# Kernel optimization log

Hardware: AMD Instinct MI355X
Metric: run time of the kernel (lower is better)

Reference implementation:

```python
import jax, jax.numpy as jnp
import numpy as np

NUM_HEADS = 32
HEAD_DIM = 64
ROPE_THETA = 10000.0


def _rope_cos_sin(position_ids, head_dim, theta):
    # inv_freq: [head_dim/2]
    half = head_dim // 2
    inv_freq = 1.0 / (theta ** (jnp.arange(0, half, dtype=jnp.float32) * 2.0 / head_dim))
    angles = position_ids.astype(jnp.float32)[..., None] * inv_freq  # [B,S,half]
    return jnp.cos(angles), jnp.sin(angles)


def _apply_rope(x, cos, sin):
    # x: [B,S,H,hd]; cos/sin: [B,S,half] -> broadcast over heads (rotate-half, Llama style)
    half = x.shape[-1] // 2
    x1, x2 = x[..., :half], x[..., half:]
    c = cos[:, :, None, :]
    s = sin[:, :, None, :]
    return jnp.concatenate([x1 * c - x2 * s, x2 * c + x1 * s], axis=-1)


def setup_inputs() -> dict:
    key = jax.random.key(0)
    ks = jax.random.split(key, 8)
    B, S, D = 2, 2048, 2048
    hidden_states = jax.random.normal(ks[0], (B, S, D), dtype=jnp.float32)
    # causal additive mask (is_causal=False in IpexSDP; mask carries causality)
    causal = jnp.tril(jnp.ones((S, S), dtype=jnp.bool_))
    attention_mask = jnp.where(causal, 0.0, -1e9).astype(jnp.float32)[None, None, :, :]
    attention_mask = jnp.broadcast_to(attention_mask, (B, 1, S, S))
    position_ids = jnp.broadcast_to(jnp.arange(S, dtype=jnp.int64)[None, :], (B, S))
    scale = 0.02
    qkv_w = jax.random.normal(ks[1], (3, D, D), dtype=jnp.float32) * scale
    qkv_b = jax.random.normal(ks[2], (3, D), dtype=jnp.float32) * scale
    o_w = jax.random.normal(ks[3], (D, D), dtype=jnp.float32) * scale
    o_b = jax.random.normal(ks[4], (D,), dtype=jnp.float32) * scale
    residual = jax.random.normal(ks[5], (B, S, D), dtype=jnp.float32)
    return {
        'hidden_states': hidden_states,
        'attention_mask': attention_mask,
        'position_ids': position_ids,
        'qkv_w': qkv_w,
        'qkv_b': qkv_b,
        'o_w': o_w,
        'o_b': o_b,
        'residual': residual,
    }


def reference(hidden_states, attention_mask, position_ids, qkv_w, qkv_b, o_w, o_b, residual):
    B, S, D = hidden_states.shape
    H, hd = NUM_HEADS, HEAD_DIM
    # fused QKV projection (weights stored transposed: x @ W), matching mm_qkv_out
    qkv = jnp.einsum('bsd,tde->tbse', hidden_states, qkv_w) + qkv_b[:, None, None, :]
    q = qkv[0].reshape(B, S, H, hd)
    k = qkv[1].reshape(B, S, H, hd)
    v = qkv[2].reshape(B, S, H, hd)
    cos, sin = _rope_cos_sin(position_ids, hd, ROPE_THETA)
    q = _apply_rope(q, cos, sin)
    k = _apply_rope(k, cos, sin)
    scale = 1.0 / jnp.sqrt(jnp.asarray(hd, dtype=hidden_states.dtype))
    # [B,H,S,S]
    scores = jnp.einsum('bqhd,bkhd->bhqk', q, k) * scale + attention_mask
    probs = jax.nn.softmax(scores, axis=-1)
    attn = jnp.einsum('bhqk,bkhd->bqhd', probs, v).reshape(B, S, D)
    # o-proj fused with bias + residual add (matmul_add_add)
    out = attn @ o_w + o_b + residual
    return out
```

## Files before the change

kernel.cpp:

```cpp
#include <hip/hip_runtime.h>
#include <stdint.h>
#include <stdio.h>

#define D_MODEL 2048
#define SEQ     2048
#define NHEADS  32
#define HDIM    64
#define BATCH   2
#define BH      (BATCH * NHEADS)
#define GK      2048

typedef unsigned short u16;
typedef unsigned int   u32;
typedef __attribute__((ext_vector_type(8))) short short8;
typedef __attribute__((ext_vector_type(4))) short s16x4;
typedef __attribute__((ext_vector_type(4))) float f32x4;
typedef __attribute__((ext_vector_type(4))) u32   u32x4;
typedef __attribute__((ext_vector_type(2))) u32   u32x2;

__device__ __forceinline__ float bf2f(u16 x) {
  union { u32 u; float f; } c; c.u = ((u32)x) << 16; return c.f;
}
__device__ __forceinline__ u16 f2bf(float f) {
  union { float f; u32 u; } c; c.f = f;
  u32 u = c.u;
  return (u16)((u + 0x7FFFu + ((u >> 16) & 1u)) >> 16);
}
__device__ __forceinline__ u32 fbits(float f) {
  union { float f; u32 u; } c; c.f = f; return c.u;
}

typedef const __attribute__((address_space(1))) u32* gas_t;
typedef __attribute__((address_space(3))) u32* las_t;
__device__ __forceinline__ void gll16(const void* g, void* l) {
  __builtin_amdgcn_global_load_lds((gas_t)g, (las_t)l, 16, 0, 0);
}

__device__ __forceinline__ void swiz_mn(int pid, int nx, int& mtile, int& ntile) {
  int chunk = 8 * nx;
  int grp = pid / chunk, loc = pid - grp * chunk;
  mtile = grp * 8 + (loc & 7);
  ntile = loc >> 3;
}

__global__ __launch_bounds__(256) void cvt_k(const float* __restrict__ in,
                                             u16* __restrict__ out) {
  int id = blockIdx.x * 256 + threadIdx.x;
  f32x4 v = *(const f32x4*)&in[(size_t)id * 4];
  alignas(8) u16 o[4];
#pragma unroll
  for (int j = 0; j < 4; j++) o[j] = f2bf(v[j]);
  *(u32x2*)&out[(size_t)id * 4] = *(const u32x2*)o;
}

__global__ __launch_bounds__(256) void transpose_cvt_k(const float* __restrict__ qkv_w,
                                                       const float* __restrict__ o_w,
                                                       u16* __restrict__ outT) {
  __shared__ u16 tile[64][72];
  const int z = blockIdx.z;
  const float* inz = (z < 3) ? qkv_w + (size_t)z * D_MODEL * D_MODEL : o_w;
  u16* outz = outT + (size_t)z * D_MODEL * D_MODEL;
  const int r0 = blockIdx.y * 64, c0 = blockIdx.x * 64;
  const int t = threadIdx.x;
  const int lrow = t >> 4, lcol4 = (t & 15) * 4;
#pragma unroll
  for (int i = 0; i < 4; i++) {
    int r = lrow + i * 16;
    f32x4 v = *(const f32x4*)&inz[(size_t)(r0 + r) * D_MODEL + (c0 + lcol4)];
#pragma unroll
    for (int j = 0; j < 4; j++) tile[r][lcol4 + j] = f2bf(v[j]);
  }
  __syncthreads();
  const int row = t >> 3, col8 = (t & 7) * 8;
#pragma unroll
  for (int i = 0; i < 2; i++) {
    int r = row + i * 32;
    alignas(16) u16 vals[8];
#pragma unroll
    for (int j = 0; j < 8; j++) vals[j] = tile[col8 + j][r];
    *(u32x4*)&outz[(size_t)(c0 + r) * D_MODEL + (r0 + col8)] = *(const u32x4*)vals;
  }
}

__device__ __forceinline__ void gemm128(const u16* __restrict__ A, const u16* __restrict__ BT,
                                        int m0, int n0, u16* As, u16* Bs, f32x4 acc[4][4]) {
  const int t = threadIdx.x;
  const int lane = t & 63, w = t >> 6;
  const int quad = lane >> 4, l16 = lane & 15;
  const int wr = w >> 1, wc = w & 1;
  const int ldr = lane >> 2, ldc = (lane & 3) * 8;
#pragma unroll
  for (int mt = 0; mt < 4; mt++)
#pragma unroll
    for (int nt = 0; nt < 4; nt++)
#pragma unroll
      for (int i = 0; i < 4; i++) acc[mt][nt][i] = 0.0f;

  for (int k0 = 0; k0 < GK; k0 += 32) {
    __syncthreads();
#pragma unroll
    for (int i = 0; i < 2; i++) {
      int rbase = w * 32 + i * 16;
      gll16(&A[(size_t)(m0 + rbase + ldr) * GK + k0 + ldc], &As[rbase * 32]);
      gll16(&BT[(size_t)(n0 + rbase + ldr) * GK + k0 + ldc], &Bs[rbase * 32]);
    }
    __syncthreads();
    short8 af[4], bf[4];
#pragma unroll
    for (int mt = 0; mt < 4; mt++)
      af[mt] = *(const short8*)&As[(wr * 64 + mt * 16 + l16) * 32 + quad * 8];
#pragma unroll
    for (int nt = 0; nt < 4; nt++)
      bf[nt] = *(const short8*)&Bs[(wc * 64 + nt * 16 + l16) * 32 + quad * 8];
#pragma unroll
    for (int mt = 0; mt < 4; mt++)
#pragma unroll
      for (int nt = 0; nt < 4; nt++)
        acc[mt][nt] = __builtin_amdgcn_mfma_f32_16x16x32_bf16(af[mt], bf[nt], acc[mt][nt], 0, 0, 0);
  }
}

__global__ __launch_bounds__(256) void qkv_gemm_k(const u16* __restrict__ A, const u16* __restrict__ BT,
                                                  const float* __restrict__ bias,
                                                  u16* __restrict__ Qb, u16* __restrict__ Kb,
                                                  u16* __restrict__ Vbt) {
  __shared__ u16 As[128 * 32], Bs[128 * 32];
  f32x4 acc[4][4];
  int mtile, ntile;
  swiz_mn(blockIdx.x, 48, mtile, ntile);
  const int m0 = mtile * 128, n0 = ntile * 128;
  gemm128(A, BT, m0, n0, As, Bs, acc);
  const int t = threadIdx.x, lane = t & 63, quad = lane >> 4, l16 = lane & 15;
  const int w = t >> 6, wr = w >> 1, wc = w & 1;
  const int tsel = n0 >> 11;

  if (tsel < 2) {
    u16* dst = tsel ? Kb : Qb;
#pragma unroll
    for (int p = 0; p < 2; p++) {
      int nlo = n0 + wc * 64 + p * 16 + l16;
      float blo = bias[nlo], bhi = bias[nlo + 32];
      int j = p * 16 + l16;
      float inv = __expf((float)j * -0.28782313662425572f);
      int h = (nlo & 2047) >> 6;
#pragma unroll
      for (int mt = 0; mt < 4; mt++) {
#pragma unroll
        for (int r = 0; r < 4; r++) {
          int m = m0 + wr * 64 + mt * 16 + quad * 4 + r;
          int b = m >> 11, s = m & (SEQ - 1);
          float sn, cs;
          __sincosf((float)s * inv, &sn, &cs);
          float x1 = acc[mt][p][r] + blo;
          float x2 = acc[mt][p + 2][r] + bhi;
          size_t base = ((size_t)((b * NHEADS + h) * SEQ + s)) * HDIM;
          dst[base + j]      = f2bf(x1 * cs - x2 * sn);
          dst[base + j + 32] = f2bf(x2 * cs + x1 * sn);
        }
      }
    }
  } else {
#pragma unroll
    for (int nt = 0; nt < 4; nt++) {
      int n = n0 + wc * 64 + nt * 16 + l16;
      float bv = bias[n];
      int e = n & 2047, h = e >> 6, d = e & 63;
#pragma unroll
      for (int mt = 0; mt < 4; mt++) {
        int m0r = m0 + wr * 64 + mt * 16 + quad * 4;
        int b = m0r >> 11, s0 = m0r & (SEQ - 1);
        alignas(8) u16 o4[4];
#pragma unroll
        for (int r = 0; r < 4; r++) o4[r] = f2bf(acc[mt][nt][r] + bv);
        *(u32x2*)&Vbt[((size_t)((b * NHEADS + h) * HDIM + d)) * SEQ + s0] = *(const u32x2*)o4;
      }
    }
  }
}

__global__ __launch_bounds__(256) void oproj_gemm_k(const u16* __restrict__ A, const u16* __restrict__ BT,
                                                    const float* __restrict__ bias,
                                                    const float* __restrict__ resid,
                                                    float* __restrict__ out) {
  __shared__ u16 As[128 * 32], Bs[128 * 32];
  f32x4 acc[4][4];
  int mtile, ntile;
  swiz_mn(blockIdx.x, 16, mtile, ntile);
  const int m0 = mtile * 128, n0 = ntile * 128;
  gemm128(A, BT, m0, n0, As, Bs, acc);
  const int t = threadIdx.x, lane = t & 63, quad = lane >> 4, l16 = lane & 15;
  const int w = t >> 6, wr = w >> 1, wc = w & 1;
#pragma unroll
  for (int nt = 0; nt < 4; nt++) {
    int n = n0 + wc * 64 + nt * 16 + l16;
    float bv = bias[n];
#pragma unroll
    for (int mt = 0; mt < 4; mt++) {
#pragma unroll
      for (int r = 0; r < 4; r++) {
        int m = m0 + wr * 64 + mt * 16 + quad * 4 + r;
        size_t oi = (size_t)m * D_MODEL + n;
        out[oi] = acc[mt][nt][r] + bv + resid[oi];
      }
    }
  }
}

__global__ __launch_bounds__(256, 2) void attn_k(const u16* __restrict__ Qb,
                                                 const u16* __restrict__ Kb,
                                                 const u16* __restrict__ Vbt,
                                                 u16* __restrict__ attn) {
  __shared__ u16 smem[128 * 72];
  u16* Ks = smem;
  u16* Vt = smem + 64 * 72;
  const int blk = blockIdx.x;
  const int bh = blk & 63, pi = blk >> 6;
  const int b = bh >> 5, h = bh & 31;
  const int t = threadIdx.x, w = t >> 6, lane = t & 63, quad = lane >> 4, l16 = lane & 15;
  const int qbT[2] = { pi * 128, (15 - pi) * 128 };
  const int qwT[2] = { qbT[0] + w * 32, qbT[1] + w * 32 };
  const size_t bho = (size_t)bh * SEQ * HDIM;
  const size_t vbo = (size_t)bh * HDIM * SEQ;
  const int kend = qbT[1] + 128;

  short8 qf[2][2][2];
#pragma unroll
  for (int Ti = 0; Ti < 2; Ti++)
#pragma unroll
    for (int qt = 0; qt < 2; qt++)
#pragma unroll
      for (int kd = 0; kd < 2; kd++) {
        short8 v = *(const short8*)&Qb[bho + (size_t)(qwT[Ti] + qt * 16 + l16) * HDIM + kd * 32 + quad * 8];
#pragma unroll
        for (int i = 0; i < 8; i++) {
          float f = bf2f((u16)v[i]) * 0.125f;
          v[i] = (short)f2bf(f);
        }
        qf[Ti][qt][kd] = v;
      }

  f32x4 Oacc[2][4][2];
  float mrow[2][2] = {{-1e30f, -1e30f}, {-1e30f, -1e30f}};
  float lrow[2][2] = {{0.0f, 0.0f}, {0.0f, 0.0f}};
#pragma unroll
  for (int Ti = 0; Ti < 2; Ti++)
#pragma unroll
    for (int dt = 0; dt < 4; dt++)
#pragma unroll
      for (int qt = 0; qt < 2; qt++)
#pragma unroll
        for (int i = 0; i < 4; i++) Oacc[Ti][dt][qt][i] = 0.0f;

  const int srow = t >> 3, sc8 = (t & 7) * 8;
  u32x4 kreg[2], vreg[2];

#pragma unroll
  for (int j = 0; j < 2; j++) {
    kreg[j] = *(const u32x4*)&Kb[bho + (size_t)(srow + j * 32) * HDIM + sc8];
    vreg[j] = *(const u32x4*)&Vbt[vbo + (size_t)(srow + j * 32) * SEQ + sc8];
  }
#pragma unroll
  for (int j = 0; j < 2; j++) {
    *(u32x4*)&Ks[(srow + j * 32) * 72 + sc8] = kreg[j];
    *(u32x4*)&Vt[(srow + j * 32) * 72 + sc8] = vreg[j];
  }
  __syncthreads();

  for (int key0 = 0; key0 < kend; key0 += 64) {
    const int nxt = key0 + 64;
    if (nxt < kend) {
#pragma unroll
      for (int j = 0; j < 2; j++) {
        kreg[j] = *(const u32x4*)&Kb[bho + (size_t)(nxt + srow + j * 32) * HDIM + sc8];
        vreg[j] = *(const u32x4*)&Vbt[vbo + (size_t)(srow + j * 32) * SEQ + nxt + sc8];
      }
    }
#pragma unroll
    for (int Ti = 0; Ti < 2; Ti++) {
      const int qw = qwT[Ti];
      if (key0 <= qw + 31) {
        const int lim = qw + 31 - key0;
        int nkt = (lim >> 4) + 1; if (nkt > 4) nkt = 4;
        f32x4 sacc[4][2];
#pragma unroll
        for (int kt = 0; kt < 4; kt++) {
          if (kt < nkt) {
            short8 kf0 = *(const short8*)&Ks[(kt * 16 + l16) * 72 + quad * 8];
            short8 kf1 = *(const short8*)&Ks[(kt * 16 + l16) * 72 + 32 + quad * 8];
#pragma unroll
            for (int qt = 0; qt < 2; qt++) {
              f32x4 z = {0.0f, 0.0f, 0.0f, 0.0f};
              z = __builtin_amdgcn_mfma_f32_16x16x32_bf16(kf0, qf[Ti][qt][0], z, 0, 0, 0);
              z = __builtin_amdgcn_mfma_f32_16x16x32_bf16(kf1, qf[Ti][qt][1], z, 0, 0, 0);
              sacc[kt][qt] = z;
            }
          }
        }
        if (key0 + 63 > qw) {
#pragma unroll
          for (int qt = 0; qt < 2; qt++) {
            int qrow = qw + qt * 16 + l16;
#pragma unroll
            for (int kt = 0; kt < 4; kt++)
              if (kt < nkt)
#pragma unroll
                for (int r = 0; r < 4; r++)
                  if (key0 + kt * 16 + quad * 4 + r > qrow) sacc[kt][qt][r] = -1e30f;
          }
        }
        float alpha[2];
#pragma unroll
        for (int qt = 0; qt < 2; qt++) {
          float mx = -1e30f;
#pragma unroll
          for (int kt = 0; kt < 4; kt++)
            if (kt < nkt)
#pragma unroll
              for (int r = 0; r < 4; r++) mx = fmaxf(mx, sacc[kt][qt][r]);
          mx = fmaxf(mx, __shfl_xor(mx, 16));
          mx = fmaxf(mx, __shfl_xor(mx, 32));
          float mnew = fmaxf(mrow[Ti][qt], mx);
          alpha[qt] = __expf(mrow[Ti][qt] - mnew);
          mrow[Ti][qt] = mnew;
          float rsum = 0.0f;
#pragma unroll
          for (int kt = 0; kt < 4; kt++)
            if (kt < nkt)
#pragma unroll
              for (int r = 0; r < 4; r++) {
                float pv = __expf(sacc[kt][qt][r] - mnew);
                sacc[kt][qt][r] = pv;
                rsum += pv;
              }
          rsum += __shfl_xor(rsum, 16);
          rsum += __shfl_xor(rsum, 32);
          lrow[Ti][qt] = lrow[Ti][qt] * alpha[qt] + rsum;
        }
#pragma unroll
        for (int dt = 0; dt < 4; dt++)
#pragma unroll
          for (int qt = 0; qt < 2; qt++)
#pragma unroll
            for (int r = 0; r < 4; r++) Oacc[Ti][dt][qt][r] *= alpha[qt];
#pragma unroll
        for (int kt = 0; kt < 4; kt++) {
          if (kt < nkt) {
            s16x4 pk[2];
#pragma unroll
            for (int qt = 0; qt < 2; qt++) {
              u32 a0 = fbits(sacc[kt][qt][0]) + 0x8000u;
              u32 a1 = fbits(sacc[kt][qt][1]) + 0x8000u;
              u32 a2 = fbits(sacc[kt][qt][2]) + 0x8000u;
              u32 a3 = fbits(sacc[kt][qt][3]) + 0x8000u;
              union { u32 u[2]; s16x4 s; } pc;
              pc.u[0] = __builtin_amdgcn_perm(a1, a0, 0x07060302u);
              pc.u[1] = __builtin_amdgcn_perm(a3, a2, 0x07060302u);
              pk[qt] = pc.s;
            }
            s16x4 vf[4];
#pragma unroll
            for (int dt = 0; dt < 4; dt++)
              vf[dt] = *(const s16x4*)&Vt[(dt * 16 + l16) * 72 + kt * 16 + quad * 4];
#pragma unroll
            for (int dt = 0; dt < 4; dt++)
#pragma unroll
              for (int qt = 0; qt < 2; qt++)
                Oacc[Ti][dt][qt] = __builtin_amdgcn_mfma_f32_16x16x16bf16_1k(vf[dt], pk[qt], Oacc[Ti][dt][qt], 0, 0, 0);
          }
        }
      }
    }
    __syncthreads();
    if (nxt < kend) {
#pragma unroll
      for (int j = 0; j < 2; j++) {
        *(u32x4*)&Ks[(srow + j * 32) * 72 + sc8] = kreg[j];
        *(u32x4*)&Vt[(srow + j * 32) * 72 + sc8] = vreg[j];
      }
      __syncthreads();
    }
  }

#pragma unroll
  for (int Ti = 0; Ti < 2; Ti++) {
    float invl[2] = {1.0f / lrow[Ti][0], 1.0f / lrow[Ti][1]};
#pragma unroll
    for (int dt = 0; dt < 4; dt++)
#pragma unroll
      for (int qt = 0; qt < 2; qt++)
#pragma unroll
        for (int r = 0; r < 4; r++)
          smem[(w * 32 + qt * 16 + l16) * 72 + dt * 16 + quad * 4 + r] =
              f2bf(Oacc[Ti][dt][qt][r] * invl[qt]);
    __syncthreads();
#pragma unroll
    for (int ii = 0; ii < 4; ii++) {
      int chunk = t + ii * 256;
      int row = chunk >> 3, g = chunk & 7;
      *(u32x4*)&attn[((size_t)(b * SEQ + qbT[Ti] + row)) * D_MODEL + h * 64 + g * 8] =
          *(const u32x4*)&smem[row * 72 + g * 8];
    }
    __syncthreads();
  }
}

extern "C" void kernel_launch(void* const* d_in, const int* in_sizes, int n_in,
                              void* d_out, int out_size, void* d_ws, size_t ws_size,
                              hipStream_t stream) {
  (void)in_sizes; (void)n_in; (void)out_size;
  const float* hidden = (const float*)d_in[0];
  const float* qkv_w = (const float*)d_in[3];
  const float* qkv_b = (const float*)d_in[4];
  const float* o_w   = (const float*)d_in[5];
  const float* o_b   = (const float*)d_in[6];
  const float* resid = (const float*)d_in[7];
  float* out = (float*)d_out;

  u16* ws = (u16*)d_ws;
  size_t off = 0;
  u16* hidb  = ws + off; off += (size_t)BATCH * SEQ * D_MODEL;
  u16* qkvT  = ws + off; off += (size_t)3 * D_MODEL * D_MODEL;
  u16* owT   = ws + off; off += (size_t)D_MODEL * D_MODEL;
  u16* Qb    = ws + off; off += (size_t)BH * SEQ * HDIM;
  u16* Kb    = ws + off; off += (size_t)BH * SEQ * HDIM;
  u16* Vbt   = ws + off; off += (size_t)BH * SEQ * HDIM;
  u16* attnb = ws + off; off += (size_t)BATCH * SEQ * D_MODEL;
  if (ws_size < off * sizeof(u16)) {
    fprintf(stderr, "kernel_launch: workspace too small: need %zu bytes, have %zu\n",
            off * sizeof(u16), ws_size);
    return;
  }
  (void)owT;

  cvt_k<<<(BATCH * SEQ * D_MODEL) / (4 * 256), 256, 0, stream>>>(hidden, hidb);
  transpose_cvt_k<<<dim3(32, 32, 4), 256, 0, stream>>>(qkv_w, o_w, qkvT);
  qkv_gemm_k<<<48 * 32, 256, 0, stream>>>(hidb, qkvT, qkv_b, Qb, Kb, Vbt);
  attn_k<<<BH * 8, 256, 0, stream>>>(Qb, Kb, Vbt, attnb);
  oproj_gemm_k<<<16 * 32, 256, 0, stream>>>(attnb, owT, o_b, resid, out);
}
```

Baseline: 443.1 us.

## Rewrite QKV GEMM with 256x256 tiles, double-buffered swizzled LDS and interleaved loads

Replaces the 128x128 QKV projection GEMM with a 512-thread kernel computing 256x256 output tiles at K-step 64. LDS is double-buffered and XOR-swizzled, and global-to-LDS loads for the next tiles are interleaved with four MFMA phases under s_setprio and barriers. The aim is more data reuse per LDS byte, fewer bank conflicts and loads overlapped with compute. The cost is 128KB of LDS and one block per CU, and the grid shrinks to 384 blocks, which may not fill all CUs evenly. The RoPE and V-transpose epilogue is adapted to the new fragment layout.

```diff
diff --git a/kernel.cpp b/kernel.cpp
--- a/kernel.cpp
+++ b/kernel.cpp
@@ -120,20 +120,136 @@
   }
 }
 
-__global__ __launch_bounds__(256) void qkv_gemm_k(const u16* __restrict__ A, const u16* __restrict__ BT,
-                                                  const float* __restrict__ bias,
-                                                  u16* __restrict__ Qb, u16* __restrict__ Kb,
-                                                  u16* __restrict__ Vbt) {
-  __shared__ u16 As[128 * 32], Bs[128 * 32];
-  f32x4 acc[4][4];
+
+__device__ __forceinline__ short8 lds_frag(const u16* tile, int row, int kh, int quad) {
+  int off = row * 128 + ((kh * 64 + quad * 16) ^ ((row & 4) << 3));
+  return *(const short8*)((const char*)tile + off);
+}
+
+__device__ __forceinline__ void stage_half(const u16* __restrict__ src, int rowbase, int k0,
+                                           u16* tile, int h, int w, int srl, int scol) {
+  u16* ldsb = tile + h * (128 * 64);
+  const u16* g0 = &src[(size_t)(rowbase + h * 128 + srl) * GK + k0 + scol];
+  const u16* g1 = &src[(size_t)(rowbase + h * 128 + srl + 8) * GK + k0 + scol];
+  gll16(g0, (char*)ldsb + w * 2048);
+  gll16(g1, (char*)ldsb + w * 2048 + 1024);
+}
+
+__global__ __launch_bounds__(512, 1) void qkv_gemm256_k(const u16* __restrict__ A,
+                                                        const u16* __restrict__ BT,
+                                                        const float* __restrict__ bias,
+                                                        u16* __restrict__ Qb, u16* __restrict__ Kb,
+                                                        u16* __restrict__ Vbt) {
+  __shared__ u16 As[2][256 * 64];
+  __shared__ u16 Bs[2][256 * 64];
+  const int t = threadIdx.x, w = t >> 6, lane = t & 63;
+  const int quad = lane >> 4, l16 = lane & 15;
+  const int wr = w >> 2, wc = w & 3;
   int mtile, ntile;
-  swiz_mn(blockIdx.x, 48, mtile, ntile);
-  const int m0 = mtile * 128, n0 = ntile * 128;
-  gemm128(A, BT, m0, n0, As, Bs, acc);
-  const int t = threadIdx.x, lane = t & 63, quad = lane >> 4, l16 = lane & 15;
-  const int w = t >> 6, wr = w >> 1, wc = w & 1;
+  swiz_mn(blockIdx.x, 24, mtile, ntile);
+  const int m0 = mtile * 256, n0 = ntile * 256;
+  const int srl = w * 16 + (lane >> 3);
+  const int scol = ((((lane & 7) * 16) ^ (((lane >> 5) & 1) << 5))) >> 1;
+
+  f32x4 acc[8][4];
+#pragma unroll
+  for (int mf = 0; mf < 8; mf++)
+#pragma unroll
+    for (int nf = 0; nf < 4; nf++)
+#pragma unroll
+      for (int i = 0; i < 4; i++) acc[mf][nf][i] = 0.0f;
+
+  const int NT = GK / 64;
+  stage_half(A, m0, 0, As[0], 0, w, srl, scol);
+  stage_half(A, m0, 0, As[0], 1, w, srl, scol);
+  stage_half(BT, n0, 0, Bs[0], 0, w, srl, scol);
+  stage_half(BT, n0, 0, Bs[0], 1, w, srl, scol);
+  stage_half(A, m0, 64, As[1], 0, w, srl, scol);
+  stage_half(A, m0, 64, As[1], 1, w, srl, scol);
+  asm volatile("s_waitcnt vmcnt(4)" ::: "memory");
+  __builtin_amdgcn_s_barrier();
+
+  for (int kt = 0; kt < NT; kt++) {
+    const int cur = kt & 1;
+    const u16* Ac = As[cur];
+    const u16* Bc = Bs[cur];
+    short8 af[8][2], bf[4][2];
+#pragma unroll
+    for (int mf = 0; mf < 4; mf++) {
+      af[mf][0] = lds_frag(Ac, wr * 128 + mf * 16 + l16, 0, quad);
+      af[mf][1] = lds_frag(Ac, wr * 128 + mf * 16 + l16, 1, quad);
+    }
+#pragma unroll
+    for (int nf = 0; nf < 2; nf++) {
+      bf[nf][0] = lds_frag(Bc, wc * 64 + nf * 16 + l16, 0, quad);
+      bf[nf][1] = lds_frag(Bc, wc * 64 + nf * 16 + l16, 1, quad);
+    }
+    if (kt + 1 < NT) stage_half(BT, n0, (kt + 1) * 64, Bs[cur ^ 1], 0, w, srl, scol);
+    __builtin_amdgcn_s_barrier();
+    __builtin_amdgcn_s_setprio(1);
+#pragma unroll
+    for (int mf = 0; mf < 4; mf++)
+#pragma unroll
+      for (int nf = 0; nf < 2; nf++) {
+        acc[mf][nf] = __builtin_amdgcn_mfma_f32_16x16x32_bf16(af[mf][0], bf[nf][0], acc[mf][nf], 0, 0, 0);
+        acc[mf][nf] = __builtin_amdgcn_mfma_f32_16x16x32_bf16(af[mf][1], bf[nf][1], acc[mf][nf], 0, 0, 0);
+      }
+    __builtin_amdgcn_s_setprio(0);
+    __builtin_amdgcn_s_barrier();
+#pragma unroll
+    for (int mf = 4; mf < 8; mf++) {
+      af[mf][0] = lds_frag(Ac, wr * 128 + mf * 16 + l16, 0, quad);
+      af[mf][1] = lds_frag(Ac, wr * 128 + mf * 16 + l16, 1, quad);
+    }
+#pragma unroll
+    for (int nf = 2; nf < 4; nf++) {
+      bf[nf][0] = lds_frag(Bc, wc * 64 + nf * 16 + l16, 0, quad);
+      bf[nf][1] = lds_frag(Bc, wc * 64 + nf * 16 + l16, 1, quad);
+    }
+    if (kt + 1 < NT) stage_half(BT, n0, (kt + 1) * 64, Bs[cur ^ 1], 1, w, srl, scol);
+    __builtin_amdgcn_s_barrier();
+    __builtin_amdgcn_s_setprio(1);
+#pragma unroll
+    for (int mf = 4; mf < 8; mf++)
+#pragma unroll
+      for (int nf = 0; nf < 2; nf++) {
+        acc[mf][nf] = __builtin_amdgcn_mfma_f32_16x16x32_bf16(af[mf][0], bf[nf][0], acc[mf][nf], 0, 0, 0);
+        acc[mf][nf] = __builtin_amdgcn_mfma_f32_16x16x32_bf16(af[mf][1], bf[nf][1], acc[mf][nf], 0, 0, 0);
+      }
+    __builtin_amdgcn_s_setprio(0);
+    __builtin_amdgcn_s_barrier();
+    if (kt + 2 < NT) stage_half(A, m0, (kt + 2) * 64, As[cur], 0, w, srl, scol);
+    __builtin_amdgcn_s_barrier();
+    __builtin_amdgcn_s_setprio(1);
+#pragma unroll
+    for (int mf = 0; mf < 4; mf++)
+#pragma unroll
+      for (int nf = 2; nf < 4; nf++) {
+        acc[mf][nf] = __builtin_amdgcn_mfma_f32_16x16x32_bf16(af[mf][0], bf[nf][0], acc[mf][nf], 0, 0, 0);
+        acc[mf][nf] = __builtin_amdgcn_mfma_f32_16x16x32_bf16(af[mf][1], bf[nf][1], acc[mf][nf], 0, 0, 0);
+      }
+    __builtin_amdgcn_s_setprio(0);
+    __builtin_amdgcn_s_barrier();
+    if (kt + 2 < NT) stage_half(A, m0, (kt + 2) * 64, As[cur], 1, w, srl, scol);
+    __builtin_amdgcn_s_barrier();
+    __builtin_amdgcn_s_setprio(1);
+#pragma unroll
+    for (int mf = 4; mf < 8; mf++)
+#pragma unroll
+      for (int nf = 2; nf < 4; nf++) {
+        acc[mf][nf] = __builtin_amdgcn_mfma_f32_16x16x32_bf16(af[mf][0], bf[nf][0], acc[mf][nf], 0, 0, 0);
+        acc[mf][nf] = __builtin_amdgcn_mfma_f32_16x16x32_bf16(af[mf][1], bf[nf][1], acc[mf][nf], 0, 0, 0);
+      }
+    __builtin_amdgcn_s_setprio(0);
+    if (kt + 2 < NT) {
+      asm volatile("s_waitcnt vmcnt(4)" ::: "memory");
+    } else {
+      asm volatile("s_waitcnt vmcnt(0)" ::: "memory");
+    }
+    __builtin_amdgcn_s_barrier();
+  }
+
   const int tsel = n0 >> 11;
-
   if (tsel < 2) {
     u16* dst = tsel ? Kb : Qb;
 #pragma unroll
@@ -144,15 +260,15 @@
       float inv = __expf((float)j * -0.28782313662425572f);
       int h = (nlo & 2047) >> 6;
 #pragma unroll
-      for (int mt = 0; mt < 4; mt++) {
+      for (int mf = 0; mf < 8; mf++) {
 #pragma unroll
         for (int r = 0; r < 4; r++) {
-          int m = m0 + wr * 64 + mt * 16 + quad * 4 + r;
+          int m = m0 + wr * 128 + mf * 16 + quad * 4 + r;
           int b = m >> 11, s = m & (SEQ - 1);
           float sn, cs;
           __sincosf((float)s * inv, &sn, &cs);
-          float x1 = acc[mt][p][r] + blo;
-          float x2 = acc[mt][p + 2][r] + bhi;
+          float x1 = acc[mf][p][r] + blo;
+          float x2 = acc[mf][p + 2][r] + bhi;
           size_t base = ((size_t)((b * NHEADS + h) * SEQ + s)) * HDIM;
           dst[base + j]      = f2bf(x1 * cs - x2 * sn);
           dst[base + j + 32] = f2bf(x2 * cs + x1 * sn);
@@ -161,17 +277,17 @@
     }
   } else {
 #pragma unroll
-    for (int nt = 0; nt < 4; nt++) {
-      int n = n0 + wc * 64 + nt * 16 + l16;
+    for (int nf = 0; nf < 4; nf++) {
+      int n = n0 + wc * 64 + nf * 16 + l16;
       float bv = bias[n];
       int e = n & 2047, h = e >> 6, d = e & 63;
 #pragma unroll
-      for (int mt = 0; mt < 4; mt++) {
-        int m0r = m0 + wr * 64 + mt * 16 + quad * 4;
+      for (int mf = 0; mf < 8; mf++) {
+        int m0r = m0 + wr * 128 + mf * 16 + quad * 4;
         int b = m0r >> 11, s0 = m0r & (SEQ - 1);
         alignas(8) u16 o4[4];
 #pragma unroll
-        for (int r = 0; r < 4; r++) o4[r] = f2bf(acc[mt][nt][r] + bv);
+        for (int r = 0; r < 4; r++) o4[r] = f2bf(acc[mf][nf][r] + bv);
         *(u32x2*)&Vbt[((size_t)((b * NHEADS + h) * HDIM + d)) * SEQ + s0] = *(const u32x2*)o4;
       }
     }
@@ -434,7 +550,7 @@
 
   cvt_k<<<(BATCH * SEQ * D_MODEL) / (4 * 256), 256, 0, stream>>>(hidden, hidb);
   transpose_cvt_k<<<dim3(32, 32, 4), 256, 0, stream>>>(qkv_w, o_w, qkvT);
-  qkv_gemm_k<<<48 * 32, 256, 0, stream>>>(hidb, qkvT, qkv_b, Qb, Kb, Vbt);
+  qkv_gemm256_k<<<16 * 24, 512, 0, stream>>>(hidb, qkvT, qkv_b, Qb, Kb, Vbt);
   attn_k<<<BH * 8, 256, 0, stream>>>(Qb, Kb, Vbt, attnb);
   oproj_gemm_k<<<16 * 32, 256, 0, stream>>>(attnb, owT, o_b, resid, out);
 }
```

Result: no change. 443.8 us (+0.2%).

## Rewrite GEMMs as 128x256 tiles with triple-buffered async LDS pipeline

Applied to the files above, without the earlier changes.

Replaces the simple 128x128, K=32 double-sync GEMM loop with a 128x256 tile on 512 threads that triple-buffers K=64 slabs through global_load_lds. It uses XOR-swizzled LDS layout, hand-scheduled ds_read_b128 with explicit waitcnt, and register double-buffered fragments. MFMA sections run at raised priority. The aim is to hide global and LDS latency and cut barrier overhead in the QKV and output projections. In exchange it uses much more LDS, allows one block per CU, and launches fewer blocks, which may leave the output projection underfilling the GPU.

```diff
diff --git a/kernel.cpp b/kernel.cpp
--- a/kernel.cpp
+++ b/kernel.cpp
@@ -9,6 +9,7 @@
 #define BATCH   2
 #define BH      (BATCH * NHEADS)
 #define GK      2048
+#define NT      (GK / 64)
 
 typedef unsigned short u16;
 typedef unsigned int   u32;
@@ -35,6 +36,17 @@
 __device__ __forceinline__ void gll16(const void* g, void* l) {
   __builtin_amdgcn_global_load_lds((gas_t)g, (las_t)l, 16, 0, 0);
 }
+__device__ __forceinline__ u32 lds_addr(const void* p) {
+  return (u32)(size_t)(const __attribute__((address_space(3))) void*)p;
+}
+template <int OFF>
+__device__ __forceinline__ short8 ds_read128o(u32 addr) {
+  short8 r;
+  asm volatile("ds_read_b128 %0, %1 offset:%2" : "=v"(r) : "v"(addr), "i"(OFF));
+  return r;
+}
+
+#define SBAR0 __builtin_amdgcn_sched_barrier(0)
 
 __device__ __forceinline__ void swiz_mn(int pid, int nx, int& mtile, int& ntile) {
   int chunk = 8 * nx;
@@ -82,58 +94,127 @@
   }
 }
 
-__device__ __forceinline__ void gemm128(const u16* __restrict__ A, const u16* __restrict__ BT,
-                                        int m0, int n0, u16* As, u16* Bs, f32x4 acc[4][4]) {
-  const int t = threadIdx.x;
-  const int lane = t & 63, w = t >> 6;
+
+__device__ __forceinline__ void stage_half(const u16* __restrict__ src, int rowbase, int k0,
+                                           u16* tile, int h, int w, int srl, int scol) {
+  u16* ldsb = tile + h * (128 * 64);
+  const u16* g0 = &src[(size_t)(rowbase + h * 128 + srl) * GK + k0 + scol];
+  const u16* g1 = &src[(size_t)(rowbase + h * 128 + srl + 8) * GK + k0 + scol];
+  gll16(g0, (char*)ldsb + w * 2048);
+  gll16(g1, (char*)ldsb + w * 2048 + 1024);
+}
+
+__device__ __forceinline__ void rd8(short8 dst[4][2], u32 base, u32 cq0, u32 cq1) {
+  u32 b0 = base + cq0, b1 = base + cq1;
+  dst[0][0] = ds_read128o<0>(b0);    dst[0][1] = ds_read128o<0>(b1);
+  dst[1][0] = ds_read128o<2048>(b0); dst[1][1] = ds_read128o<2048>(b1);
+  dst[2][0] = ds_read128o<4096>(b0); dst[2][1] = ds_read128o<4096>(b1);
+  dst[3][0] = ds_read128o<6144>(b0); dst[3][1] = ds_read128o<6144>(b1);
+}
+
+template <int NFLO>
+__device__ __forceinline__ void mfma_half(const short8 afc[4][2], const short8 bfc[4][2],
+                                          f32x4 acc[4][4]) {
+  __builtin_amdgcn_s_setprio(1);
+#pragma unroll
+  for (int mf = 0; mf < 4; mf++)
+#pragma unroll
+    for (int nf = NFLO; nf < NFLO + 2; nf++) {
+      acc[mf][nf] = __builtin_amdgcn_mfma_f32_16x16x32_bf16(afc[mf][0], bfc[nf][0], acc[mf][nf], 0, 0, 0);
+      acc[mf][nf] = __builtin_amdgcn_mfma_f32_16x16x32_bf16(afc[mf][1], bfc[nf][1], acc[mf][nf], 0, 0, 0);
+    }
+  __builtin_amdgcn_s_setprio(0);
+}
+
+#define KT_BODY(KT_, AFC, BFC, AFN, BFN)                                        \
+  do {                                                                           \
+    if ((KT_) + 1 < NT) rd8(AFN, asb + (u32)ri * (u32)(128 * 64 * 2) + rowA, cq0, cq1); \
+    if ((KT_) + 1 < NT) { asm volatile("s_waitcnt lgkmcnt(8)"); }                \
+    else                { asm volatile("s_waitcnt lgkmcnt(0)"); }                \
+    SBAR0;                                                                       \
+    mfma_half<0>(AFC, BFC, acc);                                                 \
+    if ((KT_) + 1 < NT) rd8(BFN, bsb + (u32)ri * (u32)(256 * 64 * 2) + rowB, cq0, cq1); \
+    SBAR0;                                                                       \
+    mfma_half<2>(AFC, BFC, acc);                                                 \
+    __builtin_amdgcn_s_barrier();                                                \
+    SBAR0;                                                                       \
+    if ((KT_) + 3 < NT) {                                                        \
+      const int k3_ = ((KT_) + 3) * 64;                                          \
+      stage_half(Ag, m0, k3_, AsB + si * (128 * 64), 0, w, srl, scol);           \
+      stage_half(Bg, n0, k3_, BsB + si * (256 * 64), 0, w, srl, scol);           \
+      stage_half(Bg, n0, k3_, BsB + si * (256 * 64), 1, w, srl, scol);           \
+      asm volatile("s_waitcnt vmcnt(6)");                                        \
+    } else {                                                                     \
+      asm volatile("s_waitcnt vmcnt(0)");                                        \
+    }                                                                            \
+    SBAR0;                                                                       \
+    __builtin_amdgcn_s_barrier();                                                \
+    SBAR0;                                                                       \
+    { int th_ = 3 - si - ri; si = ri; ri = th_; }                                \
+  } while (0)
+
+__device__ __forceinline__ void gemm_128x256(const u16* __restrict__ Ag,
+                                             const u16* __restrict__ Bg,
+                                             int m0, int n0,
+                                             u16* AsB, u16* BsB,
+                                             f32x4 acc[4][4]) {
+  const int t = threadIdx.x, w = t >> 6, lane = t & 63;
   const int quad = lane >> 4, l16 = lane & 15;
-  const int wr = w >> 1, wc = w & 1;
-  const int ldr = lane >> 2, ldc = (lane & 3) * 8;
-#pragma unroll
-  for (int mt = 0; mt < 4; mt++)
-#pragma unroll
-    for (int nt = 0; nt < 4; nt++)
-#pragma unroll
-      for (int i = 0; i < 4; i++) acc[mt][nt][i] = 0.0f;
-
-  for (int k0 = 0; k0 < GK; k0 += 32) {
-    __syncthreads();
-#pragma unroll
-    for (int i = 0; i < 2; i++) {
-      int rbase = w * 32 + i * 16;
-      gll16(&A[(size_t)(m0 + rbase + ldr) * GK + k0 + ldc], &As[rbase * 32]);
-      gll16(&BT[(size_t)(n0 + rbase + ldr) * GK + k0 + ldc], &Bs[rbase * 32]);
-    }
-    __syncthreads();
-    short8 af[4], bf[4];
-#pragma unroll
-    for (int mt = 0; mt < 4; mt++)
-      af[mt] = *(const short8*)&As[(wr * 64 + mt * 16 + l16) * 32 + quad * 8];
-#pragma unroll
-    for (int nt = 0; nt < 4; nt++)
-      bf[nt] = *(const short8*)&Bs[(wc * 64 + nt * 16 + l16) * 32 + quad * 8];
-#pragma unroll
-    for (int mt = 0; mt < 4; mt++)
-#pragma unroll
-      for (int nt = 0; nt < 4; nt++)
-        acc[mt][nt] = __builtin_amdgcn_mfma_f32_16x16x32_bf16(af[mt], bf[nt], acc[mt][nt], 0, 0, 0);
-  }
-}
-
-__global__ __launch_bounds__(256) void qkv_gemm_k(const u16* __restrict__ A, const u16* __restrict__ BT,
-                                                  const float* __restrict__ bias,
-                                                  u16* __restrict__ Qb, u16* __restrict__ Kb,
-                                                  u16* __restrict__ Vbt) {
-  __shared__ u16 As[128 * 32], Bs[128 * 32];
+  const int wr = w >> 2, wc = w & 3;
+  const int srl = w * 16 + (lane >> 3);
+  const int scol = (((lane & 7) ^ (lane >> 3)) << 3);
+  const u32 asb = lds_addr(AsB), bsb = lds_addr(BsB);
+  const u32 xorc = (u32)((l16 & 7) << 4);
+  const u32 cq0 = (u32)(quad * 16) ^ xorc;
+  const u32 cq1 = (u32)(64 + quad * 16) ^ xorc;
+  const u32 rowA = (u32)((wr * 64 + l16) * 128);
+  const u32 rowB = (u32)((wc * 64 + l16) * 128);
+
+#pragma unroll
+  for (int mf = 0; mf < 4; mf++)
+#pragma unroll
+    for (int nf = 0; nf < 4; nf++)
+#pragma unroll
+      for (int i = 0; i < 4; i++) acc[mf][nf][i] = 0.0f;
+
+#pragma unroll
+  for (int tt = 0; tt < 3; tt++) {
+    stage_half(Ag, m0, tt * 64, AsB + tt * (128 * 64), 0, w, srl, scol);
+    stage_half(Bg, n0, tt * 64, BsB + tt * (256 * 64), 0, w, srl, scol);
+    stage_half(Bg, n0, tt * 64, BsB + tt * (256 * 64), 1, w, srl, scol);
+  }
+  asm volatile("s_waitcnt vmcnt(6)");
+  SBAR0;
+  __builtin_amdgcn_s_barrier();
+  SBAR0;
+
+  short8 af0[4][2], bf0[4][2], af1[4][2], bf1[4][2];
+  rd8(af0, asb + rowA, cq0, cq1);
+  rd8(bf0, bsb + rowB, cq0, cq1);
+  int si = 0, ri = 1;
+
+  for (int kt = 0; kt < NT; kt += 2) {
+    KT_BODY(kt,     af0, bf0, af1, bf1);
+    KT_BODY(kt + 1, af1, bf1, af0, bf0);
+  }
+}
+
+__global__ __launch_bounds__(512, 1) void qkv_gemm_k(const u16* __restrict__ A,
+                                                     const u16* __restrict__ BT,
+                                                     const float* __restrict__ bias,
+                                                     u16* __restrict__ Qb, u16* __restrict__ Kb,
+                                                     u16* __restrict__ Vbt) {
+  __shared__ u16 As[3][128 * 64];
+  __shared__ u16 Bs[3][256 * 64];
   f32x4 acc[4][4];
   int mtile, ntile;
-  swiz_mn(blockIdx.x, 48, mtile, ntile);
-  const int m0 = mtile * 128, n0 = ntile * 128;
-  gemm128(A, BT, m0, n0, As, Bs, acc);
+  swiz_mn(blockIdx.x, 24, mtile, ntile);
+  const int m0 = mtile * 128, n0 = ntile * 256;
+  gemm_128x256(A, BT, m0, n0, &As[0][0], &Bs[0][0], acc);
+
   const int t = threadIdx.x, lane = t & 63, quad = lane >> 4, l16 = lane & 15;
-  const int w = t >> 6, wr = w >> 1, wc = w & 1;
+  const int w = t >> 6, wr = w >> 2, wc = w & 3;
   const int tsel = n0 >> 11;
-
   if (tsel < 2) {
     u16* dst = tsel ? Kb : Qb;
 #pragma unroll
@@ -144,15 +225,15 @@
       float inv = __expf((float)j * -0.28782313662425572f);
       int h = (nlo & 2047) >> 6;
 #pragma unroll
-      for (int mt = 0; mt < 4; mt++) {
+      for (int mf = 0; mf < 4; mf++) {
 #pragma unroll
         for (int r = 0; r < 4; r++) {
-          int m = m0 + wr * 64 + mt * 16 + quad * 4 + r;
+          int m = m0 + wr * 64 + mf * 16 + quad * 4 + r;
           int b = m >> 11, s = m & (SEQ - 1);
           float sn, cs;
           __sincosf((float)s * inv, &sn, &cs);
-          float x1 = acc[mt][p][r] + blo;
-          float x2 = acc[mt][p + 2][r] + bhi;
+          float x1 = acc[mf][p][r] + blo;
+          float x2 = acc[mf][p + 2][r] + bhi;
           size_t base = ((size_t)((b * NHEADS + h) * SEQ + s)) * HDIM;
           dst[base + j]      = f2bf(x1 * cs - x2 * sn);
           dst[base + j + 32] = f2bf(x2 * cs + x1 * sn);
@@ -161,46 +242,49 @@
     }
   } else {
 #pragma unroll
-    for (int nt = 0; nt < 4; nt++) {
-      int n = n0 + wc * 64 + nt * 16 + l16;
+    for (int nf = 0; nf < 4; nf++) {
+      int n = n0 + wc * 64 + nf * 16 + l16;
       float bv = bias[n];
       int e = n & 2047, h = e >> 6, d = e & 63;
 #pragma unroll
-      for (int mt = 0; mt < 4; mt++) {
-        int m0r = m0 + wr * 64 + mt * 16 + quad * 4;
+      for (int mf = 0; mf < 4; mf++) {
+        int m0r = m0 + wr * 64 + mf * 16 + quad * 4;
         int b = m0r >> 11, s0 = m0r & (SEQ - 1);
         alignas(8) u16 o4[4];
 #pragma unroll
-        for (int r = 0; r < 4; r++) o4[r] = f2bf(acc[mt][nt][r] + bv);
+        for (int r = 0; r < 4; r++) o4[r] = f2bf(acc[mf][nf][r] + bv);
         *(u32x2*)&Vbt[((size_t)((b * NHEADS + h) * HDIM + d)) * SEQ + s0] = *(const u32x2*)o4;
       }
     }
   }
 }
 
-__global__ __launch_bounds__(256) void oproj_gemm_k(const u16* __restrict__ A, const u16* __restrict__ BT,
-                                                    const float* __restrict__ bias,
-                                                    const float* __restrict__ resid,
-                                                    float* __restrict__ out) {
-  __shared__ u16 As[128 * 32], Bs[128 * 32];
+__global__ __launch_bounds__(512, 1) void oproj_gemm_k(const u16* __restrict__ A,
+                                                       const u16* __restrict__ BT,
+                                                       const float* __restrict__ bias,
+                                                       const float* __restrict__ resid,
+                                                       float* __restrict__ out) {
+  __shared__ u16 As[3][128 * 64];
+  __shared__ u16 Bs[3][256 * 64];
   f32x4 acc[4][4];
   int mtile, ntile;
-  swiz_mn(blockIdx.x, 16, mtile, ntile);
-  const int m0 = mtile * 128, n0 = ntile * 128;
-  gemm128(A, BT, m0, n0, As, Bs, acc);
+  swiz_mn(blockIdx.x, 8, mtile, ntile);
+  const int m0 = mtile * 128, n0 = ntile * 256;
+  gemm_128x256(A, BT, m0, n0, &As[0][0], &Bs[0][0], acc);
+
   const int t = threadIdx.x, lane = t & 63, quad = lane >> 4, l16 = lane & 15;
-  const int w = t >> 6, wr = w >> 1, wc = w & 1;
-#pragma unroll
-  for (int nt = 0; nt < 4; nt++) {
-    int n = n0 + wc * 64 + nt * 16 + l16;
+  const int w = t >> 6, wr = w >> 2, wc = w & 3;
+#pragma unroll
+  for (int nf = 0; nf < 4; nf++) {
+    int n = n0 + wc * 64 + nf * 16 + l16;
     float bv = bias[n];
 #pragma unroll
-    for (int mt = 0; mt < 4; mt++) {
+    for (int mf = 0; mf < 4; mf++) {
 #pragma unroll
       for (int r = 0; r < 4; r++) {
-        int m = m0 + wr * 64 + mt * 16 + quad * 4 + r;
+        int m = m0 + wr * 64 + mf * 16 + quad * 4 + r;
         size_t oi = (size_t)m * D_MODEL + n;
-        out[oi] = acc[mt][nt][r] + bv + resid[oi];
+        out[oi] = acc[mf][nf][r] + bv + resid[oi];
       }
     }
   }
@@ -434,7 +518,7 @@
 
   cvt_k<<<(BATCH * SEQ * D_MODEL) / (4 * 256), 256, 0, stream>>>(hidden, hidb);
   transpose_cvt_k<<<dim3(32, 32, 4), 256, 0, stream>>>(qkv_w, o_w, qkvT);
-  qkv_gemm_k<<<48 * 32, 256, 0, stream>>>(hidb, qkvT, qkv_b, Qb, Kb, Vbt);
+  qkv_gemm_k<<<32 * 24, 512, 0, stream>>>(hidb, qkvT, qkv_b, Qb, Kb, Vbt);
   attn_k<<<BH * 8, 256, 0, stream>>>(Qb, Kb, Vbt, attnb);
-  oproj_gemm_k<<<16 * 32, 256, 0, stream>>>(attnb, owT, o_b, resid, out);
-}
+  oproj_gemm_k<<<32 * 8, 512, 0, stream>>>(attnb, owT, o_b, resid, out);
+}
```

New measurement: 415.6 us. 1.07x faster.
